# Optimization experiments

Measured on AMD Instinct MI355X. Metric: run time of the kernel, lower is better.

## Reference

```python
import jax, jax.numpy as jnp
import numpy as np

N_NODES = 100000
N_EDGES = 1600000
IN_CH = 128
OUT_CH = 64


def setup_inputs() -> dict:
    key = jax.random.key(0)
    k1, k2, k3 = jax.random.split(key, 3)
    x = jax.random.normal(k1, (N_NODES, IN_CH), dtype=jnp.float32)
    edge_index = jax.random.randint(k2, (2, N_EDGES), 0, N_NODES, dtype=jnp.int32)
    # Glorot-style init for the GCN weight
    W = jax.random.normal(k3, (IN_CH, OUT_CH), dtype=jnp.float32) * (1.0 / np.sqrt(IN_CH))
    b = jnp.zeros((OUT_CH,), dtype=jnp.float32)
    return {"x": x, "edge_index": edge_index, "W": W, "b": b}


def reference(x, edge_index, W, b):
    # GCNConv (PyG semantics): linear transform, add self loops,
    # symmetric deg^{-1/2} normalization, scatter-add aggregation, bias; then ReLU.
    n = x.shape[0]
    h = x @ W  # [N, out]

    loops = jnp.arange(n, dtype=edge_index.dtype)
    row = jnp.concatenate([edge_index[0], loops])  # source nodes
    col = jnp.concatenate([edge_index[1], loops])  # target nodes

    deg = jax.ops.segment_sum(jnp.ones_like(col, dtype=h.dtype), col, num_segments=n)
    deg_inv_sqrt = jnp.where(deg > 0, jax.lax.rsqrt(jnp.maximum(deg, 1e-12)), 0.0)
    norm = deg_inv_sqrt[row] * deg_inv_sqrt[col]  # [E+N]

    msg = h[row] * norm[:, None]  # gather + scale
    out = jax.ops.segment_sum(msg, col, num_segments=n)  # scatter-add
    return jax.nn.relu(out + b)
```

## Files before the change

kernel.cpp:

```cpp
#include <hip/hip_runtime.h>
#include <hip/hip_fp16.h>

#define INC 128
#define OUTC 64
#define MAXBUK 512
#define CAP 6144
#define FCH 3200

typedef __attribute__((ext_vector_type(8))) short short8;
typedef __attribute__((ext_vector_type(4))) float f32x4;

__device__ __forceinline__ ushort f2bf(float f) {
    union { float f; unsigned u; } v; v.f = f;
    unsigned r = v.u + 0x7FFF + ((v.u >> 16) & 1);
    return (ushort)(r >> 16);
}

__global__ __launch_bounds__(512) void buk_fill_kernel(const int* __restrict__ rowi,
                                                       const int* __restrict__ coli,
                                                       int* __restrict__ cursor,
                                                       int* __restrict__ packed,
                                                       int E, int nbuk, int per) {
    __shared__ int lcnt[512];
    __shared__ int lbase[512];
    __shared__ int wsum[8];
    __shared__ int sp[FCH];
    __shared__ ushort sb[FCH];
    int tid = threadIdx.x;
    int lane = tid & 63, w = tid >> 6;
    int c0 = blockIdx.x * per;
    int c1 = min(E, c0 + per);
    lcnt[tid] = 0;
    __syncthreads();

    int es[7], ed[7];
    int ne = 0;
    for (int e = c0 + tid; e < c1; e += 512) {
        int s = rowi[e], d = coli[e];
        es[ne] = s; ed[ne] = d; ne++;
        atomicAdd(&lcnt[d >> 8], 1);
    }
    __syncthreads();

    int v = lcnt[tid];
    int x = v;
    #pragma unroll
    for (int off = 1; off < 64; off <<= 1) {
        int t = __shfl_up(x, off);
        if (lane >= off) x += t;
    }
    if (lane == 63) wsum[w] = x;
    __syncthreads();
    if (w == 0) {
        int t = (lane < 8) ? wsum[lane] : 0;
        #pragma unroll
        for (int off = 1; off < 8; off <<= 1) {
            int u = __shfl_up(t, off);
            if (lane >= off) t += u;
        }
        if (lane < 8) wsum[lane] = t;
    }
    __syncthreads();
    int ex = x + (w ? wsum[w - 1] : 0) - v;
    int gb = 0;
    if (v) gb = atomicAdd(&cursor[tid], v);
    lbase[tid] = gb - ex;
    lcnt[tid] = ex;
    __syncthreads();

    for (int i = 0; i < ne; ++i) {
        int d = ed[i];
        int bk = d >> 8;
        int pos = atomicAdd(&lcnt[bk], 1);
        sp[pos] = (es[i] << 8) | (d & 255);
        sb[pos] = (ushort)bk;
    }
    __syncthreads();

    int m = c1 - c0;
    for (int t = tid; t < m; t += 512) {
        int bk = sb[t];
        int p = lbase[bk] + t;
        if (p < CAP)
            packed[(size_t)bk * CAP + p] = sp[t];
    }
}

#define WT_STRIDE 136
__global__ __launch_bounds__(256) void gemm_kernel(
        const float* __restrict__ x, const float* __restrict__ W,
        const int* __restrict__ packed, const int* __restrict__ cursor,
        __half2* __restrict__ g2, int n) {
    __shared__ ushort WT[OUTC * WT_STRIDE];
    __shared__ int cnt[128];
    int tid = threadIdx.x;
    if (tid < 128) cnt[tid] = 0;
    #pragma unroll
    for (int i = 0; i < 8; ++i) {
        int idx4 = tid + i * 256;
        float4 v = ((const float4*)W)[idx4];
        int e = idx4 * 4;
        int k = e >> 6, nn = e & 63;
        WT[(nn + 0) * WT_STRIDE + k] = f2bf(v.x);
        WT[(nn + 1) * WT_STRIDE + k] = f2bf(v.y);
        WT[(nn + 2) * WT_STRIDE + k] = f2bf(v.z);
        WT[(nn + 3) * WT_STRIDE + k] = f2bf(v.w);
    }
    __syncthreads();

    int rbase = blockIdx.x * 128;
    int bucket = rbase >> 8;
    int off = rbase & 255;

    {
        int m = min(cursor[bucket], CAP);
        const int* pk = packed + (size_t)bucket * CAP;
        for (int e = tid; e < m; e += 256) {
            int r = (pk[e] & 255) - off;
            if ((unsigned)r < 128u) atomicAdd(&cnt[r], 1);
        }
    }

    int w = tid >> 6, lane = tid & 63;
    int m = lane & 15, quad = lane >> 4;
    int rw = rbase + w * 32;

    short8 afrag[2][4];
    #pragma unroll
    for (int rt = 0; rt < 2; ++rt) {
        int row = rw + rt * 16 + m;
        #pragma unroll
        for (int kc = 0; kc < 4; ++kc) {
            float4 v0 = make_float4(0.f, 0.f, 0.f, 0.f), v1 = v0;
            if (row < n) {
                const float* p = x + (size_t)row * INC + kc * 32 + quad * 8;
                v0 = *(const float4*)p;
                v1 = *(const float4*)(p + 4);
            }
            short8 a;
            a[0] = (short)f2bf(v0.x); a[1] = (short)f2bf(v0.y);
            a[2] = (short)f2bf(v0.z); a[3] = (short)f2bf(v0.w);
            a[4] = (short)f2bf(v1.x); a[5] = (short)f2bf(v1.y);
            a[6] = (short)f2bf(v1.z); a[7] = (short)f2bf(v1.w);
            afrag[rt][kc] = a;
        }
    }

    f32x4 acc[2][4];
    #pragma unroll
    for (int rt = 0; rt < 2; ++rt)
        #pragma unroll
        for (int nt = 0; nt < 4; ++nt)
            acc[rt][nt] = (f32x4){0.f, 0.f, 0.f, 0.f};

    #pragma unroll
    for (int nt = 0; nt < 4; ++nt) {
        #pragma unroll
        for (int kc = 0; kc < 4; ++kc) {
            short8 bf = *(const short8*)&WT[(nt * 16 + m) * WT_STRIDE + kc * 32 + quad * 8];
            acc[0][nt] = __builtin_amdgcn_mfma_f32_16x16x32_bf16(afrag[0][kc], bf, acc[0][nt], 0, 0, 0);
            acc[1][nt] = __builtin_amdgcn_mfma_f32_16x16x32_bf16(afrag[1][kc], bf, acc[1][nt], 0, 0, 0);
        }
    }

    __syncthreads();

    #pragma unroll
    for (int rt = 0; rt < 2; ++rt) {
        #pragma unroll
        for (int reg = 0; reg < 4; ++reg) {
            int r2 = rw + rt * 16 + quad * 4 + reg;
            if (r2 < n) {
                float di = rsqrtf(1.0f + (float)cnt[r2 - rbase]);
                #pragma unroll
                for (int nt = 0; nt < 2; ++nt)
                    g2[(size_t)r2 * 32 + nt * 16 + m] =
                        __floats2half2_rn(acc[rt][nt][reg] * di, acc[rt][nt + 2][reg] * di);
            }
        }
    }
}

__global__ __launch_bounds__(1024) void agg_kernel(const int* __restrict__ packed,
                                                   const int* __restrict__ cursor,
                                                   const __half2* __restrict__ g2,
                                                   const float* __restrict__ b,
                                                   float* __restrict__ out, int n) {
    __shared__ int cnt[256];
    __shared__ int sc[256];
    __shared__ int cur[256];
    __shared__ int lcsr[CAP];
    int k = blockIdx.x, tid = threadIdx.x;
    int r0 = k << 8;
    if (tid < 256) cnt[tid] = 0;
    __syncthreads();
    int m = min(cursor[k], CAP);
    const int* pk = packed + (size_t)k * CAP;
    int pe[(CAP + 1023) / 1024];
    int ne = 0;
    for (int e = tid; e < m; e += 1024) {
        int p = pk[e];
        pe[ne++] = p;
        atomicAdd(&cnt[p & 255], 1);
    }
    __syncthreads();
    int c = (tid < 256) ? cnt[tid] : 0;
    if (tid < 256) sc[tid] = c;
    __syncthreads();
    #pragma unroll
    for (int off = 1; off < 256; off <<= 1) {
        int t = (tid >= off && tid < 256) ? sc[tid - off] : 0;
        __syncthreads();
        if (tid < 256) sc[tid] += t;
        __syncthreads();
    }
    if (tid < 256) cur[tid] = sc[tid] - c;
    __syncthreads();
    for (int i = 0; i < ne; ++i) {
        int p = pe[i];
        int pos = atomicAdd(&cur[p & 255], 1);
        lcsr[pos] = (int)(((unsigned)p) >> 8);
    }
    __syncthreads();

    int w = tid >> 6, lane = tid & 63;
    int l = lane & 31, half = lane >> 5;
    const __half2* gl = g2 + l;
    float bx = b[l], by = b[l + 32];
    for (int cl = w; cl < 256; cl += 16) {
        int e1 = sc[cl];
        int nd = cnt[cl];
        int j = e1 - nd;
        float ax = 0.f, ay = 0.f;
        for (; j + 16 <= e1; j += 16) {
            int s0 = lcsr[j + half];
            int s1 = lcsr[j + 2 + half];
            int s2 = lcsr[j + 4 + half];
            int s3 = lcsr[j + 6 + half];
            int s4 = lcsr[j + 8 + half];
            int s5 = lcsr[j + 10 + half];
            int s6 = lcsr[j + 12 + half];
            int s7 = lcsr[j + 14 + half];
            float2 f0 = __half22float2(gl[(size_t)s0 * 32]);
            float2 f1 = __half22float2(gl[(size_t)s1 * 32]);
            float2 f2 = __half22float2(gl[(size_t)s2 * 32]);
            float2 f3 = __half22float2(gl[(size_t)s3 * 32]);
            float2 f4 = __half22float2(gl[(size_t)s4 * 32]);
            float2 f5 = __half22float2(gl[(size_t)s5 * 32]);
            float2 f6 = __half22float2(gl[(size_t)s6 * 32]);
            float2 f7 = __half22float2(gl[(size_t)s7 * 32]);
            ax += ((f0.x + f1.x) + (f2.x + f3.x)) + ((f4.x + f5.x) + (f6.x + f7.x));
            ay += ((f0.y + f1.y) + (f2.y + f3.y)) + ((f4.y + f5.y) + (f6.y + f7.y));
        }
        if (j + 8 <= e1) {
            int s0 = lcsr[j + half];
            int s1 = lcsr[j + 2 + half];
            int s2 = lcsr[j + 4 + half];
            int s3 = lcsr[j + 6 + half];
            float2 f0 = __half22float2(gl[(size_t)s0 * 32]);
            float2 f1 = __half22float2(gl[(size_t)s1 * 32]);
            float2 f2 = __half22float2(gl[(size_t)s2 * 32]);
            float2 f3 = __half22float2(gl[(size_t)s3 * 32]);
            ax += (f0.x + f1.x) + (f2.x + f3.x);
            ay += (f0.y + f1.y) + (f2.y + f3.y);
            j += 8;
        }
        for (; j + 2 <= e1; j += 2) {
            int s = lcsr[j + half];
            float2 f = __half22float2(gl[(size_t)s * 32]);
            ax += f.x; ay += f.y;
        }
        if (j < e1 && half == 0) {
            int s = lcsr[j];
            float2 f = __half22float2(gl[(size_t)s * 32]);
            ax += f.x; ay += f.y;
        }
        ax += __shfl_xor(ax, 32);
        ay += __shfl_xor(ay, 32);
        int node = r0 + cl;
        if (half == 0 && node < n) {
            float2 s = __half22float2(gl[(size_t)node * 32]);
            float di = rsqrtf(1.0f + (float)nd);
            out[(size_t)node * OUTC + l]      = fmaxf((ax + s.x) * di + bx, 0.f);
            out[(size_t)node * OUTC + 32 + l] = fmaxf((ay + s.y) * di + by, 0.f);
        }
    }
}

extern "C" void kernel_launch(void* const* d_in, const int* in_sizes, int n_in,
                              void* d_out, int out_size, void* d_ws, size_t ws_size,
                              hipStream_t stream) {
    const float* x  = (const float*)d_in[0];
    const int*   ei = (const int*)d_in[1];
    const float* W  = (const float*)d_in[2];
    const float* b  = (const float*)d_in[3];
    float* out = (float*)d_out;

    int n = in_sizes[0] / INC;
    int E = in_sizes[1] / 2;
    const int* rowi = ei;
    const int* coli = ei + E;

    int nbuk = (n + 255) >> 8;

    char* ws = (char*)d_ws;
    int*     cursor = (int*)ws;                  ws += (size_t)MAXBUK * 4;
    int*     packed = (int*)ws;                  ws += (size_t)nbuk * CAP * 4;
    __half2* g2     = (__half2*)ws;

    int fblocks = 512;
    int per = (E + fblocks - 1) / fblocks;

    (void)hipMemsetAsync(cursor, 0, (size_t)MAXBUK * 4, stream);
    buk_fill_kernel<<<fblocks, 512, 0, stream>>>(rowi, coli, cursor, packed, E, nbuk, per);
    gemm_kernel<<<(n + 127) / 128, 256, 0, stream>>>(x, W, packed, cursor, g2, n);
    agg_kernel<<<nbuk, 1024, 0, stream>>>(packed, cursor, g2, b, out, n);
}
```

Before: 169.0 us.

## Fuse bucket fill, GEMM and aggregation into one cooperative persistent kernel

Replaces the memset plus three kernel launches with a single cooperative kernel of nbuk blocks (512 threads each), separated by grid-wide syncs, and shares LDS through a union. Each block now bins one chunk of edges (a larger per-block chunk and FCH), computes the GEMM for 256 rows, and aggregates one bucket. The aim is to remove launch gaps and the memset. The cost is grid.sync overhead, and only ~391 blocks of 512 threads run where the aggregation stage used 1024 threads before, which may reduce latency hiding in the gather-heavy stage. The old path is kept as a fallback if the cooperative launch fails.

```diff
diff --git a/kernel.cpp b/kernel.cpp
--- a/kernel.cpp
+++ b/kernel.cpp
@@ -1,11 +1,14 @@
 #include <hip/hip_runtime.h>
 #include <hip/hip_fp16.h>
+#include <hip/hip_cooperative_groups.h>
+
+namespace cg = cooperative_groups;
 
 #define INC 128
 #define OUTC 64
 #define MAXBUK 512
 #define CAP 6144
-#define FCH 3200
+#define FCH 4224
 
 typedef __attribute__((ext_vector_type(8))) short short8;
 typedef __attribute__((ext_vector_type(4))) float f32x4;
@@ -14,6 +17,283 @@
     union { float f; unsigned u; } v; v.f = f;
     unsigned r = v.u + 0x7FFF + ((v.u >> 16) & 1);
     return (ushort)(r >> 16);
+}
+
+#define WT_STRIDE 136
+
+union SMem {
+    struct {
+        int lcnt[512];
+        int lbase[512];
+        int wsum[8];
+        int sp[FCH];
+        ushort sb[FCH];
+    } fill;
+    struct {
+        ushort WT[OUTC * WT_STRIDE];
+        int cnt[256];
+    } gemm;
+    struct {
+        int cnt[256];
+        int sc[256];
+        int cur[256];
+        int lcsr[CAP];
+    } agg;
+};
+
+__global__ __launch_bounds__(512, 4) void fused_kernel(
+        const int* __restrict__ rowi, const int* __restrict__ coli,
+        const float* __restrict__ x, const float* __restrict__ W,
+        const float* __restrict__ b, float* __restrict__ out,
+        int* __restrict__ cursor, int* __restrict__ packed,
+        __half2* __restrict__ g2, int n, int E, int per) {
+    __shared__ SMem sm;
+    cg::grid_group grid = cg::this_grid();
+    int k = blockIdx.x, tid = threadIdx.x;
+    int lane = tid & 63, w = tid >> 6;
+
+    if (k == 0) cursor[tid] = 0;
+    grid.sync();
+
+    {
+        int c0 = k * per;
+        int c1 = min(E, c0 + per);
+        sm.fill.lcnt[tid] = 0;
+        __syncthreads();
+
+        int es[8], ed[8];
+        int ne = 0;
+        for (int e = c0 + tid; e < c1; e += 512) {
+            int s = rowi[e], d = coli[e];
+            es[ne] = s; ed[ne] = d; ne++;
+            atomicAdd(&sm.fill.lcnt[d >> 8], 1);
+        }
+        __syncthreads();
+
+        int v = sm.fill.lcnt[tid];
+        int xx = v;
+        #pragma unroll
+        for (int off = 1; off < 64; off <<= 1) {
+            int t = __shfl_up(xx, off);
+            if (lane >= off) xx += t;
+        }
+        if (lane == 63) sm.fill.wsum[w] = xx;
+        __syncthreads();
+        if (w == 0) {
+            int t = (lane < 8) ? sm.fill.wsum[lane] : 0;
+            #pragma unroll
+            for (int off = 1; off < 8; off <<= 1) {
+                int u = __shfl_up(t, off);
+                if (lane >= off) t += u;
+            }
+            if (lane < 8) sm.fill.wsum[lane] = t;
+        }
+        __syncthreads();
+        int ex = xx + (w ? sm.fill.wsum[w - 1] : 0) - v;
+        int gb = 0;
+        if (v) gb = atomicAdd(&cursor[tid], v);
+        sm.fill.lbase[tid] = gb - ex;
+        sm.fill.lcnt[tid] = ex;
+        __syncthreads();
+
+        for (int i = 0; i < ne; ++i) {
+            int d = ed[i];
+            int bk = d >> 8;
+            int pos = atomicAdd(&sm.fill.lcnt[bk], 1);
+            sm.fill.sp[pos] = (es[i] << 8) | (d & 255);
+            sm.fill.sb[pos] = (ushort)bk;
+        }
+        __syncthreads();
+        int m = c1 - c0;
+        for (int t = tid; t < m; t += 512) {
+            int bk = sm.fill.sb[t];
+            int p = sm.fill.lbase[bk] + t;
+            if (p < CAP)
+                packed[(size_t)bk * CAP + p] = sm.fill.sp[t];
+        }
+    }
+    __threadfence();
+    grid.sync();
+
+    {
+        if (tid < 256) sm.gemm.cnt[tid] = 0;
+        #pragma unroll
+        for (int i = 0; i < 4; ++i) {
+            int idx4 = tid + i * 512;
+            float4 v = ((const float4*)W)[idx4];
+            int e = idx4 * 4;
+            int kk = e >> 6, nn = e & 63;
+            sm.gemm.WT[(nn + 0) * WT_STRIDE + kk] = f2bf(v.x);
+            sm.gemm.WT[(nn + 1) * WT_STRIDE + kk] = f2bf(v.y);
+            sm.gemm.WT[(nn + 2) * WT_STRIDE + kk] = f2bf(v.z);
+            sm.gemm.WT[(nn + 3) * WT_STRIDE + kk] = f2bf(v.w);
+        }
+        __syncthreads();
+
+        int r0 = k << 8;
+        {
+            int m = min(cursor[k], CAP);
+            const int* pk = packed + (size_t)k * CAP;
+            for (int e = tid; e < m; e += 512)
+                atomicAdd(&sm.gemm.cnt[pk[e] & 255], 1);
+        }
+
+        int mm = lane & 15, quad = lane >> 4;
+        int rw = r0 + w * 32;
+
+        short8 afrag[2][4];
+        #pragma unroll
+        for (int rt = 0; rt < 2; ++rt) {
+            int row = rw + rt * 16 + mm;
+            #pragma unroll
+            for (int kc = 0; kc < 4; ++kc) {
+                float4 v0 = make_float4(0.f, 0.f, 0.f, 0.f), v1 = v0;
+                if (row < n) {
+                    const float* p = x + (size_t)row * INC + kc * 32 + quad * 8;
+                    v0 = *(const float4*)p;
+                    v1 = *(const float4*)(p + 4);
+                }
+                short8 a;
+                a[0] = (short)f2bf(v0.x); a[1] = (short)f2bf(v0.y);
+                a[2] = (short)f2bf(v0.z); a[3] = (short)f2bf(v0.w);
+                a[4] = (short)f2bf(v1.x); a[5] = (short)f2bf(v1.y);
+                a[6] = (short)f2bf(v1.z); a[7] = (short)f2bf(v1.w);
+                afrag[rt][kc] = a;
+            }
+        }
+
+        f32x4 acc[2][4];
+        #pragma unroll
+        for (int rt = 0; rt < 2; ++rt)
+            #pragma unroll
+            for (int nt = 0; nt < 4; ++nt)
+                acc[rt][nt] = (f32x4){0.f, 0.f, 0.f, 0.f};
+
+        #pragma unroll
+        for (int nt = 0; nt < 4; ++nt) {
+            #pragma unroll
+            for (int kc = 0; kc < 4; ++kc) {
+                short8 bf = *(const short8*)&sm.gemm.WT[(nt * 16 + mm) * WT_STRIDE + kc * 32 + quad * 8];
+                acc[0][nt] = __builtin_amdgcn_mfma_f32_16x16x32_bf16(afrag[0][kc], bf, acc[0][nt], 0, 0, 0);
+                acc[1][nt] = __builtin_amdgcn_mfma_f32_16x16x32_bf16(afrag[1][kc], bf, acc[1][nt], 0, 0, 0);
+            }
+        }
+
+        __syncthreads();
+
+        #pragma unroll
+        for (int rt = 0; rt < 2; ++rt) {
+            #pragma unroll
+            for (int reg = 0; reg < 4; ++reg) {
+                int r2 = rw + rt * 16 + quad * 4 + reg;
+                if (r2 < n) {
+                    float di = rsqrtf(1.0f + (float)sm.gemm.cnt[r2 - r0]);
+                    #pragma unroll
+                    for (int nt = 0; nt < 2; ++nt)
+                        g2[(size_t)r2 * 32 + nt * 16 + mm] =
+                            __floats2half2_rn(acc[rt][nt][reg] * di, acc[rt][nt + 2][reg] * di);
+                }
+            }
+        }
+    }
+    __threadfence();
+    grid.sync();
+
+    {
+        int r0 = k << 8;
+        if (tid < 256) sm.agg.cnt[tid] = 0;
+        __syncthreads();
+        int m = min(cursor[k], CAP);
+        const int* pk = packed + (size_t)k * CAP;
+        int pe[(CAP + 511) / 512];
+        int ne = 0;
+        for (int e = tid; e < m; e += 512) {
+            int p = pk[e];
+            pe[ne++] = p;
+            atomicAdd(&sm.agg.cnt[p & 255], 1);
+        }
+        __syncthreads();
+        int c = (tid < 256) ? sm.agg.cnt[tid] : 0;
+        if (tid < 256) sm.agg.sc[tid] = c;
+        __syncthreads();
+        #pragma unroll
+        for (int off = 1; off < 256; off <<= 1) {
+            int t = (tid >= off && tid < 256) ? sm.agg.sc[tid - off] : 0;
+            __syncthreads();
+            if (tid < 256) sm.agg.sc[tid] += t;
+            __syncthreads();
+        }
+        if (tid < 256) sm.agg.cur[tid] = sm.agg.sc[tid] - c;
+        __syncthreads();
+        for (int i = 0; i < ne; ++i) {
+            int p = pe[i];
+            int pos = atomicAdd(&sm.agg.cur[p & 255], 1);
+            sm.agg.lcsr[pos] = (int)(((unsigned)p) >> 8);
+        }
+        __syncthreads();
+
+        int l = lane & 31, half = lane >> 5;
+        const __half2* gl = g2 + l;
+        float bx = b[l], by = b[l + 32];
+        for (int cl = w; cl < 256; cl += 8) {
+            int e1 = sm.agg.sc[cl];
+            int nd = sm.agg.cnt[cl];
+            int j = e1 - nd;
+            float ax = 0.f, ay = 0.f;
+            for (; j + 16 <= e1; j += 16) {
+                int s0 = sm.agg.lcsr[j + half];
+                int s1 = sm.agg.lcsr[j + 2 + half];
+                int s2 = sm.agg.lcsr[j + 4 + half];
+                int s3 = sm.agg.lcsr[j + 6 + half];
+                int s4 = sm.agg.lcsr[j + 8 + half];
+                int s5 = sm.agg.lcsr[j + 10 + half];
+                int s6 = sm.agg.lcsr[j + 12 + half];
+                int s7 = sm.agg.lcsr[j + 14 + half];
+                float2 f0 = __half22float2(gl[(size_t)s0 * 32]);
+                float2 f1 = __half22float2(gl[(size_t)s1 * 32]);
+                float2 f2 = __half22float2(gl[(size_t)s2 * 32]);
+                float2 f3 = __half22float2(gl[(size_t)s3 * 32]);
+                float2 f4 = __half22float2(gl[(size_t)s4 * 32]);
+                float2 f5 = __half22float2(gl[(size_t)s5 * 32]);
+                float2 f6 = __half22float2(gl[(size_t)s6 * 32]);
+                float2 f7 = __half22float2(gl[(size_t)s7 * 32]);
+                ax += ((f0.x + f1.x) + (f2.x + f3.x)) + ((f4.x + f5.x) + (f6.x + f7.x));
+                ay += ((f0.y + f1.y) + (f2.y + f3.y)) + ((f4.y + f5.y) + (f6.y + f7.y));
+            }
+            if (j + 8 <= e1) {
+                int s0 = sm.agg.lcsr[j + half];
+                int s1 = sm.agg.lcsr[j + 2 + half];
+                int s2 = sm.agg.lcsr[j + 4 + half];
+                int s3 = sm.agg.lcsr[j + 6 + half];
+                float2 f0 = __half22float2(gl[(size_t)s0 * 32]);
+                float2 f1 = __half22float2(gl[(size_t)s1 * 32]);
+                float2 f2 = __half22float2(gl[(size_t)s2 * 32]);
+                float2 f3 = __half22float2(gl[(size_t)s3 * 32]);
+                ax += (f0.x + f1.x) + (f2.x + f3.x);
+                ay += (f0.y + f1.y) + (f2.y + f3.y);
+                j += 8;
+            }
+            for (; j + 2 <= e1; j += 2) {
+                int s = sm.agg.lcsr[j + half];
+                float2 f = __half22float2(gl[(size_t)s * 32]);
+                ax += f.x; ay += f.y;
+            }
+            if (j < e1 && half == 0) {
+                int s = sm.agg.lcsr[j];
+                float2 f = __half22float2(gl[(size_t)s * 32]);
+                ax += f.x; ay += f.y;
+            }
+            ax += __shfl_xor(ax, 32);
+            ay += __shfl_xor(ay, 32);
+            int node = r0 + cl;
+            if (half == 0 && node < n) {
+                float2 s = __half22float2(gl[(size_t)node * 32]);
+                float di = rsqrtf(1.0f + (float)nd);
+                out[(size_t)node * OUTC + l]      = fmaxf((ax + s.x) * di + bx, 0.f);
+                out[(size_t)node * OUTC + 32 + l] = fmaxf((ay + s.y) * di + by, 0.f);
+            }
+        }
+    }
 }
 
 __global__ __launch_bounds__(512) void buk_fill_kernel(const int* __restrict__ rowi,
@@ -32,8 +312,7 @@
     int c1 = min(E, c0 + per);
     lcnt[tid] = 0;
     __syncthreads();
-
-    int es[7], ed[7];
+    int es[8], ed[8];
     int ne = 0;
     for (int e = c0 + tid; e < c1; e += 512) {
         int s = rowi[e], d = coli[e];
@@ -41,7 +320,6 @@
         atomicAdd(&lcnt[d >> 8], 1);
     }
     __syncthreads();
-
     int v = lcnt[tid];
     int x = v;
     #pragma unroll
@@ -67,7 +345,6 @@
     lbase[tid] = gb - ex;
     lcnt[tid] = ex;
     __syncthreads();
-
     for (int i = 0; i < ne; ++i) {
         int d = ed[i];
         int bk = d >> 8;
@@ -76,7 +353,6 @@
         sb[pos] = (ushort)bk;
     }
     __syncthreads();
-
     int m = c1 - c0;
     for (int t = tid; t < m; t += 512) {
         int bk = sb[t];
@@ -86,7 +362,6 @@
     }
 }
 
-#define WT_STRIDE 136
 __global__ __launch_bounds__(256) void gemm_kernel(
         const float* __restrict__ x, const float* __restrict__ W,
         const int* __restrict__ packed, const int* __restrict__ cursor,
@@ -107,11 +382,9 @@
         WT[(nn + 3) * WT_STRIDE + k] = f2bf(v.w);
     }
     __syncthreads();
-
     int rbase = blockIdx.x * 128;
     int bucket = rbase >> 8;
     int off = rbase & 255;
-
     {
         int m = min(cursor[bucket], CAP);
         const int* pk = packed + (size_t)bucket * CAP;
@@ -120,11 +393,9 @@
             if ((unsigned)r < 128u) atomicAdd(&cnt[r], 1);
         }
     }
-
     int w = tid >> 6, lane = tid & 63;
     int m = lane & 15, quad = lane >> 4;
     int rw = rbase + w * 32;
-
     short8 afrag[2][4];
     #pragma unroll
     for (int rt = 0; rt < 2; ++rt) {
@@ -145,14 +416,12 @@
             afrag[rt][kc] = a;
         }
     }
-
     f32x4 acc[2][4];
     #pragma unroll
     for (int rt = 0; rt < 2; ++rt)
         #pragma unroll
         for (int nt = 0; nt < 4; ++nt)
             acc[rt][nt] = (f32x4){0.f, 0.f, 0.f, 0.f};
-
     #pragma unroll
     for (int nt = 0; nt < 4; ++nt) {
         #pragma unroll
@@ -162,9 +431,7 @@
             acc[1][nt] = __builtin_amdgcn_mfma_f32_16x16x32_bf16(afrag[1][kc], bf, acc[1][nt], 0, 0, 0);
         }
     }
-
-    __syncthreads();
-
+    __syncthreads();
     #pragma unroll
     for (int rt = 0; rt < 2; ++rt) {
         #pragma unroll
@@ -222,7 +489,6 @@
         lcsr[pos] = (int)(((unsigned)p) >> 8);
     }
     __syncthreads();
-
     int w = tid >> 6, lane = tid & 63;
     int l = lane & 31, half = lane >> 5;
     const __half2* gl = g2 + l;
@@ -308,11 +574,19 @@
     int*     packed = (int*)ws;                  ws += (size_t)nbuk * CAP * 4;
     __half2* g2     = (__half2*)ws;
 
-    int fblocks = 512;
-    int per = (E + fblocks - 1) / fblocks;
-
-    (void)hipMemsetAsync(cursor, 0, (size_t)MAXBUK * 4, stream);
-    buk_fill_kernel<<<fblocks, 512, 0, stream>>>(rowi, coli, cursor, packed, E, nbuk, per);
-    gemm_kernel<<<(n + 127) / 128, 256, 0, stream>>>(x, W, packed, cursor, g2, n);
-    agg_kernel<<<nbuk, 1024, 0, stream>>>(packed, cursor, g2, b, out, n);
+    int per = (E + nbuk - 1) / nbuk;
+
+    void* args[] = { (void*)&rowi, (void*)&coli, (void*)&x, (void*)&W, (void*)&b,
+                     (void*)&out, (void*)&cursor, (void*)&packed, (void*)&g2,
+                     (void*)&n, (void*)&E, (void*)&per };
+    hipError_t err = hipLaunchCooperativeKernel((const void*)fused_kernel,
+                                                dim3(nbuk), dim3(512), args, 0, stream);
+    if (err != hipSuccess) {
+        int fblocks = 512;
+        int fper = (E + fblocks - 1) / fblocks;
+        (void)hipMemsetAsync(cursor, 0, (size_t)MAXBUK * 4, stream);
+        buk_fill_kernel<<<fblocks, 512, 0, stream>>>(rowi, coli, cursor, packed, E, nbuk, fper);
+        gemm_kernel<<<(n + 127) / 128, 256, 0, stream>>>(x, W, packed, cursor, g2, n);
+        agg_kernel<<<nbuk, 1024, 0, stream>>>(packed, cursor, g2, b, out, n);
+    }
 }
```

New measurement: 493.4 us. 2.92x slower.
